# Performance work log

Measured on AMD Instinct MI355X. Metric: run time of the kernel, lower is better.

## Reference

```python
import jax, jax.numpy as jnp
import numpy as np

B, T, N, C = 8, 16, 2048, 512


def setup_inputs() -> dict:
    key = jax.random.key(0)
    k1, k2, k3, k4, k5, k6 = jax.random.split(key, 6)
    return {
        "vd_s": jax.random.normal(k1, (B, T, C), dtype=jnp.float32),
        "vd_nodes": jax.random.normal(k2, (B, N, C), dtype=jnp.float32),
        # 1x1 conv weights initialized N(0, 0.01) as in the torch module
        "W1": jax.random.normal(k3, (C, C), dtype=jnp.float32) * 0.01,
        "b1": jax.random.normal(k4, (C,), dtype=jnp.float32) * 0.01,
        "W2": jax.random.normal(k5, (C, C), dtype=jnp.float32) * 0.01,
        "b2": jax.random.normal(k6, (C,), dtype=jnp.float32) * 0.01,
    }


def reference(vd_s, vd_nodes, W1, b1, W2, b2):
    # propagation_step = 1 (as in the original module)
    def per_graph(s, nodes):
        # s: [T, C] scene features, nodes: [N, C] node features
        out_scene = s.mean(axis=0)                     # [C]
        state = nodes                                  # [N, C]
        # 1x1 convs on [N, C, 1, 1] == per-node linear layers
        mat1 = state @ W1.T + b1                       # [N, C]
        mat2 = state @ W2.T + b2                       # [N, C]
        adj = mat1 @ mat2.T                            # [N, N]
        soft_adj = jax.nn.softmax(adj, axis=1)         # row-softmax (dim=1)
        new_state = soft_adj @ state + state           # message update + residual
        gp_out = new_state.mean(axis=0)                # [C]
        return jnp.concatenate([out_scene, gp_out], axis=0)  # [2C]

    return jax.vmap(per_graph)(vd_s, vd_nodes)         # [B, 2C]
```

## Files before the change

### kernel.cpp

```cpp
#include <hip/hip_runtime.h>

typedef __bf16 bf16;
typedef __bf16 bf16x8 __attribute__((ext_vector_type(8), aligned(16)));
typedef float  f32x4  __attribute__((ext_vector_type(4)));
typedef float  f32x2  __attribute__((ext_vector_type(2)));

#define B_ 8
#define T_ 16
#define N_ 2048
#define C_ 512

__device__ inline bf16x8 load8_f32(const float* p) {
    float4 a = *(const float4*)p;
    float4 b = *(const float4*)(p + 4);
    bf16x8 r;
    r[0] = (bf16)a.x; r[1] = (bf16)a.y; r[2] = (bf16)a.z; r[3] = (bf16)a.w;
    r[4] = (bf16)b.x; r[5] = (bf16)b.y; r[6] = (bf16)b.z; r[7] = (bf16)b.w;
    return r;
}

__device__ inline void gload_lds16(const void* g, void* l) {
    __builtin_amdgcn_global_load_lds(
        (const __attribute__((address_space(1))) void*)g,
        (__attribute__((address_space(3))) void*)l, 16, 0, 0);
}

__device__ inline unsigned char f32_to_fp8(float v) {
    int p = __builtin_amdgcn_cvt_pk_fp8_f32(v, 0.f, 0, false);
    return (unsigned char)(p & 0xff);
}

__device__ inline void fp8x4_to_f32(unsigned int wd, float* o) {
    f32x2 lo = __builtin_amdgcn_cvt_pk_f32_fp8((int)wd, false);
    f32x2 hi = __builtin_amdgcn_cvt_pk_f32_fp8((int)wd, true);
    o[0] = lo[0]; o[1] = lo[1]; o[2] = hi[0]; o[3] = hi[1];
}

__global__ __launch_bounds__(256) void k_prep(
    const float* __restrict__ vd_s, const float* __restrict__ nodes,
    const float* __restrict__ W1, const float* __restrict__ W2,
    float* __restrict__ out, bf16* __restrict__ nodes_bf,
    unsigned char* __restrict__ nodes_f8,
    bf16* __restrict__ W1t, bf16* __restrict__ W2t) {
    __shared__ float sh[32 * 33];
    const int bx = blockIdx.x, tid = threadIdx.x;
    if (bx < 2048) {
        size_t i = ((size_t)bx * 256 + tid) * 16;
        float v[16];
        *(float4*)&v[0]  = *(const float4*)(nodes + i);
        *(float4*)&v[4]  = *(const float4*)(nodes + i + 4);
        *(float4*)&v[8]  = *(const float4*)(nodes + i + 8);
        *(float4*)&v[12] = *(const float4*)(nodes + i + 12);
        bf16x8 b0, b1;
#pragma unroll
        for (int e = 0; e < 8; ++e) { b0[e] = (bf16)v[e]; b1[e] = (bf16)v[8 + e]; }
        *(bf16x8*)(nodes_bf + i)     = b0;
        *(bf16x8*)(nodes_bf + i + 8) = b1;
        uint4 u;
        unsigned int wds[4];
#pragma unroll
        for (int k = 0; k < 4; ++k) {
            int p = __builtin_amdgcn_cvt_pk_fp8_f32(v[k * 4 + 0], v[k * 4 + 1], 0, false);
            p = __builtin_amdgcn_cvt_pk_fp8_f32(v[k * 4 + 2], v[k * 4 + 3], p, true);
            wds[k] = (unsigned int)p;
        }
        u.x = wds[0]; u.y = wds[1]; u.z = wds[2]; u.w = wds[3];
        *(uint4*)(nodes_f8 + i) = u;
    } else if (bx < 2064) {
        int gt = (bx - 2048) * 256 + tid;
        int b = gt >> 9, c = gt & 511;
        float s = 0.f;
#pragma unroll
        for (int t = 0; t < T_; ++t) s += vd_s[(size_t)b * T_ * C_ + t * C_ + c];
        out[b * 2 * C_ + c] = s * (1.0f / T_);
    } else {
        const float* W = (bx < 2320) ? W1 : W2;
        bf16* Wt = (bx < 2320) ? W1t : W2t;
        int idx = (bx < 2320) ? bx - 2064 : bx - 2320;
        int bxx = (idx & 15) * 32, byy = (idx >> 4) * 32;
        int tx = tid & 31, ty = tid >> 5;
#pragma unroll
        for (int r = 0; r < 32; r += 8)
            sh[(ty + r) * 33 + tx] = W[(size_t)(byy + ty + r) * C_ + bxx + tx];
        __syncthreads();
#pragma unroll
        for (int r = 0; r < 32; r += 8)
            Wt[(size_t)(bxx + ty + r) * C_ + byy + tx] = (bf16)sh[tx * 33 + ty + r];
    }
}

__global__ void k_q(const float* __restrict__ b1, const bf16* __restrict__ W2t,
                    float* __restrict__ q) {
    int wid = threadIdx.x >> 6, lane = threadIdx.x & 63;
    int c = blockIdx.x * 4 + wid;
    bf16x8 v8 = *(const bf16x8*)(W2t + (size_t)c * C_ + lane * 8);
    float s = 0.f;
#pragma unroll
    for (int i = 0; i < 8; ++i) s += (float)v8[i] * b1[lane * 8 + i];
#pragma unroll
    for (int m = 32; m; m >>= 1) s += __shfl_xor(s, m);
    if (lane == 0) q[c] = s;
}

template <int OM>
__global__ __launch_bounds__(256) void gemm_nt(
    const bf16* __restrict__ A, size_t strideA,
    const bf16* __restrict__ Bm, size_t strideB,
    const float* __restrict__ bias,
    void* __restrict__ Cv, size_t strideC,
    int N, int K) {
    __shared__ __attribute__((aligned(16))) bf16 lA[128 * 64];
    __shared__ __attribute__((aligned(16))) bf16 lB[128 * 64];
    const int tid = threadIdx.x;
    const int lane = tid & 63, w = tid >> 6;
    const int wm = w >> 1, wn = w & 1;
    const int z = blockIdx.z;
    const int bm = blockIdx.x * 128, bn = blockIdx.y * 128;
    const bf16* Ab = A + (size_t)z * strideA;
    const bf16* Bb = Bm + (size_t)z * strideB;

    f32x4 acc[4][4];
#pragma unroll
    for (int i = 0; i < 4; ++i)
#pragma unroll
        for (int j = 0; j < 4; ++j) acc[i][j] = f32x4{0.f, 0.f, 0.f, 0.f};

    const int nkt = K >> 6;
    for (int kt = 0; kt < nkt; ++kt) {
#pragma unroll
        for (int c = 0; c < 4; ++c) {
            int ca = c * 256 + tid;
            int row = ca >> 3;
            int qd = (ca & 7) ^ (row & 7);
            gload_lds16(Ab + (size_t)(bm + row) * K + kt * 64 + qd * 8,
                        lA + c * 2048 + w * 512);
            gload_lds16(Bb + (size_t)(bn + row) * K + kt * 64 + qd * 8,
                        lB + c * 2048 + w * 512);
        }
        __syncthreads();

        bf16x8 af[2][4], bfr[2][4];
#pragma unroll
        for (int ks = 0; ks < 2; ++ks) {
            int y = ks * 4 + (lane >> 4);
#pragma unroll
            for (int i = 0; i < 4; ++i) {
                int ra = wm * 64 + i * 16 + (lane & 15);
                int rb = wn * 64 + i * 16 + (lane & 15);
                af[ks][i]  = *(const bf16x8*)&lA[ra * 64 + ((y ^ (ra & 7)) * 8)];
                bfr[ks][i] = *(const bf16x8*)&lB[rb * 64 + ((y ^ (rb & 7)) * 8)];
            }
        }
#pragma unroll
        for (int ks = 0; ks < 2; ++ks)
#pragma unroll
            for (int i = 0; i < 4; ++i)
#pragma unroll
                for (int j = 0; j < 4; ++j)
                    acc[i][j] = __builtin_amdgcn_mfma_f32_16x16x32_bf16(
                        af[ks][i], bfr[ks][j], acc[i][j], 0, 0, 0);
        __syncthreads();
    }

#pragma unroll
    for (int i = 0; i < 4; ++i) {
#pragma unroll
        for (int j = 0; j < 4; ++j) {
            int col = bn + wn * 64 + j * 16 + (lane & 15);
            float bv = bias ? bias[col] : 0.f;
#pragma unroll
            for (int r = 0; r < 4; ++r) {
                int row = bm + wm * 64 + i * 16 + (lane >> 4) * 4 + r;
                float v = acc[i][j][r] + bv;
                if constexpr (OM == 0) {
                    ((bf16*)Cv)[(size_t)z * strideC + (size_t)row * N + col] = (bf16)v;
                } else {
                    ((unsigned char*)Cv)[(size_t)z * strideC + (size_t)row * N + col] =
                        f32_to_fp8(v * 16.0f);
                }
            }
        }
    }
}

__global__ __launch_bounds__(1024, 4) void gemm256w(
    const unsigned char* __restrict__ A, const unsigned char* __restrict__ Bm,
    unsigned char* __restrict__ P) {
    __shared__ __attribute__((aligned(16))) unsigned char ls[2][2][16384];
    const int tid = threadIdx.x;
    const int lane = tid & 63, w = tid >> 6;
    const int wm = w >> 2, wn = w & 3;
    const int qh = lane >> 5, ql = (lane >> 4) & 1;
    const int id = blockIdx.x;
    const int sw = (id & 7) * 64 + (id >> 3);
    const int z = sw >> 6, tt = sw & 63;
    const int bm = (tt >> 3) * 256, bn = (tt & 7) * 256;
    const unsigned char* Ab = A + (size_t)z * N_ * C_;
    const unsigned char* Bb = Bm + (size_t)z * N_ * C_;

    f32x4 acc[4][4];
#pragma unroll
    for (int i = 0; i < 4; ++i)
#pragma unroll
        for (int j = 0; j < 4; ++j) acc[i][j] = f32x4{0.f, 0.f, 0.f, 0.f};

#define STAGE_T(kt_, buf_)                                                        \
    {                                                                             \
        int row = tid >> 2;                                                       \
        int qd = (tid & 3) ^ ((row >> 1) & 3);                                    \
        gload_lds16(Ab + (size_t)(bm + row) * 512 + (kt_) * 64 + qd * 16,         \
                    &ls[buf_][0][w * 1024]);                                      \
        gload_lds16(Bb + (size_t)(bn + row) * 512 + (kt_) * 64 + qd * 16,         \
                    &ls[buf_][1][w * 1024]);                                      \
    }

    STAGE_T(0, 0);
    STAGE_T(1, 1);
    asm volatile("s_waitcnt vmcnt(2)" ::: "memory");
    __builtin_amdgcn_s_barrier();
    asm volatile("" ::: "memory");

#pragma unroll
    for (int j = 0; j < 8; ++j) {
        const int cur = j & 1;
        const unsigned char* lA = &ls[cur][0][0];
        const unsigned char* lB = &ls[cur][1][0];

        long af[4][2], bfv[4][2];
#pragma unroll
        for (int i = 0; i < 4; ++i) {
            int ra = wm * 64 + i * 16 + (lane & 15);
            int rr = (ra >> 1) & 3;
#pragma unroll
            for (int ks = 0; ks < 2; ++ks)
                af[i][ks] = *(const long*)&lA[ra * 64 + (((ks * 2 + qh) ^ rr) * 16) + ql * 8];
        }
#pragma unroll
        for (int jj = 0; jj < 4; ++jj) {
            int rb = wn * 64 + jj * 16 + (lane & 15);
            int rr = (rb >> 1) & 3;
#pragma unroll
            for (int ks = 0; ks < 2; ++ks)
                bfv[jj][ks] = *(const long*)&lB[rb * 64 + (((ks * 2 + qh) ^ rr) * 16) + ql * 8];
        }
        __builtin_amdgcn_s_setprio(1);
#pragma unroll
        for (int ks = 0; ks < 2; ++ks)
#pragma unroll
            for (int i = 0; i < 4; ++i)
#pragma unroll
                for (int jj = 0; jj < 4; ++jj)
                    acc[i][jj] = __builtin_amdgcn_mfma_f32_16x16x32_fp8_fp8(
                        af[i][ks], bfv[jj][ks], acc[i][jj], 0, 0, 0);
        __builtin_amdgcn_s_setprio(0);

        asm volatile("" ::: "memory");
        __builtin_amdgcn_s_barrier();
        asm volatile("" ::: "memory");

        if (j + 2 < 8) STAGE_T(j + 2, cur);
        if (j < 7) {
            if (j < 6) asm volatile("s_waitcnt vmcnt(2)" ::: "memory");
            else       asm volatile("s_waitcnt vmcnt(0)" ::: "memory");
            __builtin_amdgcn_s_barrier();
            asm volatile("" ::: "memory");
        }
    }

    unsigned char* Pb = P + (size_t)z * N_ * N_;
#pragma unroll
    for (int fi = 0; fi < 4; ++fi) {
#pragma unroll
        for (int fj = 0; fj < 4; ++fj) {
            int col = bn + wn * 64 + fj * 16 + (lane & 15);
#pragma unroll
            for (int r = 0; r < 4; ++r) {
                int row = bm + wm * 64 + fi * 16 + (lane >> 4) * 4 + r;
                float v = __expf(fminf(acc[fi][fj][r] * 0.0625f, 8.8f)) * 0.0625f;
                Pb[(size_t)row * N_ + col] = f32_to_fp8(v);
            }
        }
    }
#undef STAGE_T
}

__global__ __launch_bounds__(256) void k_w2(const unsigned char* __restrict__ P,
                                            float* __restrict__ wpart) {
    __shared__ float rp[16 * 256];
    __shared__ float ri[16];
    const int tid = threadIdx.x;
    const int s = blockIdx.x, b = blockIdx.y;
    const unsigned char* Pb = P + (size_t)b * N_ * N_ + (size_t)s * 16 * N_;
    const int j0 = tid * 8;
    uint2 v[16];
#pragma unroll
    for (int r = 0; r < 16; ++r) {
        v[r] = *(const uint2*)&Pb[(size_t)r * N_ + j0];
        float f[8];
        fp8x4_to_f32(v[r].x, &f[0]);
        fp8x4_to_f32(v[r].y, &f[4]);
        float t = 0.f;
#pragma unroll
        for (int e = 0; e < 8; ++e) t += f[e];
        rp[r * 256 + tid] = t;
    }
    __syncthreads();
    {
        int row = tid >> 4, seg = tid & 15;
        float t = 0.f;
#pragma unroll
        for (int k = 0; k < 16; ++k) t += rp[row * 256 + seg + 16 * k];
#pragma unroll
        for (int m = 8; m; m >>= 1) t += __shfl_xor(t, m);
        if (seg == 0) ri[row] = 1.0f / t;
    }
    __syncthreads();
    float acc8[8] = {0.f, 0.f, 0.f, 0.f, 0.f, 0.f, 0.f, 0.f};
#pragma unroll
    for (int r = 0; r < 16; ++r) {
        float rr = ri[r];
        float f[8];
        fp8x4_to_f32(v[r].x, &f[0]);
        fp8x4_to_f32(v[r].y, &f[4]);
#pragma unroll
        for (int e = 0; e < 8; ++e) acc8[e] += rr * f[e];
    }
    float* wp = wpart + ((size_t)b * 128 + s) * (size_t)N_;
#pragma unroll
    for (int e = 0; e < 8; ++e) wp[j0 + e] = acc8[e];
}

__global__ __launch_bounds__(256) void k_gp(const unsigned char* __restrict__ nodes_f8,
                                            const float* __restrict__ wpart,
                                            float* __restrict__ gppart) {
    __shared__ float wred[4][64];
    __shared__ float wsh[64];
    __shared__ float gred[4][512];
    const int tid = threadIdx.x;
    const int slab = blockIdx.x, b = blockIdx.y;
    const int jj = tid & 63, sg = tid >> 6;
    float wacc = 0.f;
    for (int s = sg; s < 128; s += 4)
        wacc += wpart[((size_t)b * 128 + s) * N_ + slab * 64 + jj];
    wred[sg][jj] = wacc;
    __syncthreads();
    if (tid < 64)
        wsh[tid] = wred[0][tid] + wred[1][tid] + wred[2][tid] + wred[3][tid] + 1.0f;
    __syncthreads();
    const int j0 = slab * 64;
    const int cc = (tid & 63) * 8, jr = tid >> 6;
    const unsigned char* nb = nodes_f8 + (size_t)b * N_ * C_;
    float acc8[8] = {0.f, 0.f, 0.f, 0.f, 0.f, 0.f, 0.f, 0.f};
    for (int j = jr; j < 64; j += 4) {
        float wj = wsh[j];
        uint2 nv = *(const uint2*)&nb[(size_t)(j0 + j) * C_ + cc];
        float f[8];
        fp8x4_to_f32(nv.x, &f[0]);
        fp8x4_to_f32(nv.y, &f[4]);
#pragma unroll
        for (int e = 0; e < 8; ++e) acc8[e] += wj * f[e];
    }
#pragma unroll
    for (int e = 0; e < 8; ++e) gred[jr][cc + e] = acc8[e];
    __syncthreads();
    if (tid < 64) {
#pragma unroll
        for (int e = 0; e < 8; ++e) {
            int c = tid * 8 + e;
            gppart[((size_t)slab * 8 + b) * C_ + c] =
                gred[0][c] + gred[1][c] + gred[2][c] + gred[3][c];
        }
    }
}

__global__ void k_fin(const float* __restrict__ gppart, float* __restrict__ out) {
    int gt = blockIdx.x * 256 + threadIdx.x;
    int b = gt >> 9, c = gt & 511;
    float s = 0.f;
#pragma unroll
    for (int k = 0; k < 32; ++k) s += gppart[((size_t)k * 8 + b) * C_ + c];
    out[b * 2 * C_ + C_ + c] = s * (1.0f / N_);
}

extern "C" void kernel_launch(void* const* d_in, const int* in_sizes, int n_in,
                              void* d_out, int out_size, void* d_ws, size_t ws_size,
                              hipStream_t stream) {
    const float* vd_s  = (const float*)d_in[0];
    const float* nodes = (const float*)d_in[1];
    const float* W1    = (const float*)d_in[2];
    const float* b1    = (const float*)d_in[3];
    const float* W2    = (const float*)d_in[4];
    float* out = (float*)d_out;

    char* ws = (char*)d_ws;
    bf16*          nodes_bf = (bf16*)(ws);
    unsigned char* H2f8     = (unsigned char*)(ws + ((size_t)16 << 20));
    float*         wpart    = (float*)(ws + ((size_t)16 << 20));
    unsigned char* nodes_f8 = (unsigned char*)(ws + ((size_t)24 << 20));
    unsigned char* P        = (unsigned char*)(ws + ((size_t)32 << 20));
    bf16*          W1t      = (bf16*)(ws + ((size_t)96 << 20));
    bf16*          W2t      = (bf16*)(ws + ((size_t)96 << 20) + (512u << 10));
    bf16*          Gt       = (bf16*)(ws + ((size_t)96 << 20) + (1024u << 10));
    char*          fbase    = ws + ((size_t)96 << 20) + (1536u << 10);
    float*         q        = (float*)(fbase);
    float*         gppart   = (float*)(fbase + 4096);

    k_prep<<<2576, 256, 0, stream>>>(vd_s, nodes, W1, W2,
                                     out, nodes_bf, nodes_f8, W1t, W2t);
    k_q<<<128, 256, 0, stream>>>(b1, W2t, q);

    gemm_nt<0><<<dim3(4, 4, 1), 256, 0, stream>>>(
        W2t, 0, W1t, 0, nullptr, Gt, 0, C_, C_);
    gemm_nt<1><<<dim3(16, 4, 8), 256, 0, stream>>>(
        nodes_bf, (size_t)N_ * C_, Gt, 0, q,
        H2f8, (size_t)N_ * C_, C_, C_);
    gemm256w<<<512, 1024, 0, stream>>>(H2f8, nodes_f8, P);

    k_w2<<<dim3(128, 8), 256, 0, stream>>>(P, wpart);
    k_gp<<<dim3(32, 8), 256, 0, stream>>>(nodes_f8, wpart, gppart);
    k_fin<<<16, 256, 0, stream>>>(gppart, out);
}
```

Measured before the change: 108.6 us.

## Permute fp8 K-layout so MFMA operands load as single 16-byte LDS reads

Changes the global byte layout of the fp8 operand matrices (nodes_f8 and the fp8 GEMM output) by permuting each 64-byte K chunk, so that the fp8 GEMM's LDS fragment loads become one 128-bit read per row instead of two 64-bit reads. The LDS XOR swizzle is adjusted to match, and the consumer kernel that reads nodes_f8 remaps its column indices to undo the permutation. This halves the LDS read instructions in the hot loop at the cost of scattered 8-byte global stores and index arithmetic in the producers.

```diff
diff --git a/kernel.cpp b/kernel.cpp
--- a/kernel.cpp
+++ b/kernel.cpp
@@ -4,21 +4,13 @@
 typedef __bf16 bf16x8 __attribute__((ext_vector_type(8), aligned(16)));
 typedef float  f32x4  __attribute__((ext_vector_type(4)));
 typedef float  f32x2  __attribute__((ext_vector_type(2)));
+typedef long   longx2 __attribute__((ext_vector_type(2)));
 
 #define B_ 8
 #define T_ 16
 #define N_ 2048
 #define C_ 512
 
-__device__ inline bf16x8 load8_f32(const float* p) {
-    float4 a = *(const float4*)p;
-    float4 b = *(const float4*)(p + 4);
-    bf16x8 r;
-    r[0] = (bf16)a.x; r[1] = (bf16)a.y; r[2] = (bf16)a.z; r[3] = (bf16)a.w;
-    r[4] = (bf16)b.x; r[5] = (bf16)b.y; r[6] = (bf16)b.z; r[7] = (bf16)b.w;
-    return r;
-}
-
 __device__ inline void gload_lds16(const void* g, void* l) {
     __builtin_amdgcn_global_load_lds(
         (const __attribute__((address_space(1))) void*)g,
@@ -35,6 +27,7 @@
     f32x2 hi = __builtin_amdgcn_cvt_pk_f32_fp8((int)wd, true);
     o[0] = lo[0]; o[1] = lo[1]; o[2] = hi[0]; o[3] = hi[1];
 }
+
 
 __global__ __launch_bounds__(256) void k_prep(
     const float* __restrict__ vd_s, const float* __restrict__ nodes,
@@ -56,7 +49,6 @@
         for (int e = 0; e < 8; ++e) { b0[e] = (bf16)v[e]; b1[e] = (bf16)v[8 + e]; }
         *(bf16x8*)(nodes_bf + i)     = b0;
         *(bf16x8*)(nodes_bf + i + 8) = b1;
-        uint4 u;
         unsigned int wds[4];
 #pragma unroll
         for (int k = 0; k < 4; ++k) {
@@ -64,8 +56,14 @@
             p = __builtin_amdgcn_cvt_pk_fp8_f32(v[k * 4 + 2], v[k * 4 + 3], p, true);
             wds[k] = (unsigned int)p;
         }
-        u.x = wds[0]; u.y = wds[1]; u.z = wds[2]; u.w = wds[3];
-        *(uint4*)(nodes_f8 + i) = u;
+        int j = (int)((i >> 4) & 3);
+        size_t base = i & ~(size_t)63;
+        size_t pa1 = base + (size_t)(((2 * j) & 3) * 16 + (j >> 1) * 8);
+        size_t pa2 = base + (size_t)(((2 * j + 1) & 3) * 16 + (j >> 1) * 8);
+        uint2 u1; u1.x = wds[0]; u1.y = wds[1];
+        uint2 u2; u2.x = wds[2]; u2.y = wds[3];
+        *(uint2*)(nodes_f8 + pa1) = u1;
+        *(uint2*)(nodes_f8 + pa2) = u2;
     } else if (bx < 2064) {
         int gt = (bx - 2048) * 256 + tid;
         int b = gt >> 9, c = gt & 511;
@@ -175,7 +173,10 @@
                 if constexpr (OM == 0) {
                     ((bf16*)Cv)[(size_t)z * strideC + (size_t)row * N + col] = (bf16)v;
                 } else {
-                    ((unsigned char*)Cv)[(size_t)z * strideC + (size_t)row * N + col] =
+                    int m = lane & 15;
+                    int colp = (col & ~63) + ((2 * j + (m >> 3)) & 3) * 16 +
+                               (j >> 1) * 8 + (m & 7);
+                    ((unsigned char*)Cv)[(size_t)z * strideC + (size_t)row * N + colp] =
                         f32_to_fp8(v * 16.0f);
                 }
             }
@@ -190,7 +191,7 @@
     const int tid = threadIdx.x;
     const int lane = tid & 63, w = tid >> 6;
     const int wm = w >> 2, wn = w & 3;
-    const int qh = lane >> 5, ql = (lane >> 4) & 1;
+    const int q4 = lane >> 4;
     const int id = blockIdx.x;
     const int sw = (id & 7) * 64 + (id >> 3);
     const int z = sw >> 6, tt = sw & 63;
@@ -207,7 +208,7 @@
 #define STAGE_T(kt_, buf_)                                                        \
     {                                                                             \
         int row = tid >> 2;                                                       \
-        int qd = (tid & 3) ^ ((row >> 1) & 3);                                    \
+        int qd = (tid & 3) ^ (row & 3);                                           \
         gload_lds16(Ab + (size_t)(bm + row) * 512 + (kt_) * 64 + qd * 16,         \
                     &ls[buf_][0][w * 1024]);                                      \
         gload_lds16(Bb + (size_t)(bn + row) * 512 + (kt_) * 64 + qd * 16,         \
@@ -230,18 +231,14 @@
 #pragma unroll
         for (int i = 0; i < 4; ++i) {
             int ra = wm * 64 + i * 16 + (lane & 15);
-            int rr = (ra >> 1) & 3;
-#pragma unroll
-            for (int ks = 0; ks < 2; ++ks)
-                af[i][ks] = *(const long*)&lA[ra * 64 + (((ks * 2 + qh) ^ rr) * 16) + ql * 8];
+            longx2 t = *(const longx2*)&lA[ra * 64 + ((q4 ^ (ra & 3)) * 16)];
+            af[i][0] = t[0]; af[i][1] = t[1];
         }
 #pragma unroll
         for (int jj = 0; jj < 4; ++jj) {
             int rb = wn * 64 + jj * 16 + (lane & 15);
-            int rr = (rb >> 1) & 3;
-#pragma unroll
-            for (int ks = 0; ks < 2; ++ks)
-                bfv[jj][ks] = *(const long*)&lB[rb * 64 + (((ks * 2 + qh) ^ rr) * 16) + ql * 8];
+            longx2 t = *(const longx2*)&lB[rb * 64 + ((q4 ^ (rb & 3)) * 16)];
+            bfv[jj][0] = t[0]; bfv[jj][1] = t[1];
         }
         __builtin_amdgcn_s_setprio(1);
 #pragma unroll
@@ -349,6 +346,7 @@
     __syncthreads();
     const int j0 = slab * 64;
     const int cc = (tid & 63) * 8, jr = tid >> 6;
+    const int lc = (cc & ~63) + ((cc >> 3) & 1) * 32 + ((cc >> 4) & 3) * 8;
     const unsigned char* nb = nodes_f8 + (size_t)b * N_ * C_;
     float acc8[8] = {0.f, 0.f, 0.f, 0.f, 0.f, 0.f, 0.f, 0.f};
     for (int j = jr; j < 64; j += 4) {
@@ -361,7 +359,7 @@
         for (int e = 0; e < 8; ++e) acc8[e] += wj * f[e];
     }
 #pragma unroll
-    for (int e = 0; e < 8; ++e) gred[jr][cc + e] = acc8[e];
+    for (int e = 0; e < 8; ++e) gred[jr][lc + e] = acc8[e];
     __syncthreads();
     if (tid < 64) {
 #pragma unroll
```

Result: no change. 106.7 us (-1.7%).
